# Kernel optimization log

Hardware: AMD Instinct MI355X
Metric: run time of the kernel (lower is better)

Reference implementation:

```python
import jax, jax.numpy as jnp
import numpy as np

DIM = 2048
N_HEADS = 32
N_KV_HEADS = 8
HEAD_DIM = DIM // N_HEADS  # 64
N_REP = N_HEADS // N_KV_HEADS
ROPE_BASE = 10000.0


def rope_tables(seq_len, dim):
    inv_freq = 1.0 / (ROPE_BASE ** (jnp.arange(0, dim, 2, dtype=jnp.float32) / dim))
    t = jnp.arange(seq_len, dtype=jnp.float32)
    freqs = jnp.outer(t, inv_freq)            # [S, dim/2]
    emb = jnp.concatenate([freqs, freqs], -1)  # [S, dim]
    return jnp.cos(emb), jnp.sin(emb)          # each [S, dim]


def rotate_half(x):
    x1, x2 = jnp.split(x, 2, axis=-1)
    return jnp.concatenate([-x2, x1], axis=-1)


def setup_inputs() -> dict:
    key = jax.random.key(0)
    k_x, k_q, k_k, k_v, k_o = jax.random.split(key, 5)
    B, S = 2, 2048
    scale = 0.02
    x = jax.random.normal(k_x, (B, S, DIM), dtype=jnp.float32)
    # torch Linear weights are [out, in]
    w_q = jax.random.normal(k_q, (N_HEADS * HEAD_DIM, DIM), dtype=jnp.float32) * scale
    w_k = jax.random.normal(k_k, (N_KV_HEADS * HEAD_DIM, DIM), dtype=jnp.float32) * scale
    w_v = jax.random.normal(k_v, (N_KV_HEADS * HEAD_DIM, DIM), dtype=jnp.float32) * scale
    w_o = jax.random.normal(k_o, (DIM, N_HEADS * HEAD_DIM), dtype=jnp.float32) * scale
    return {"x": x, "w_q": w_q, "w_k": w_k, "w_v": w_v, "w_o": w_o}


def reference(x, w_q, w_k, w_v, w_o):
    B, S, _ = x.shape
    # projections (torch Linear: x @ W^T), reshape to [B, H, S, D]
    q = jnp.einsum('bsd,ed->bse', x, w_q).reshape(B, S, N_HEADS, HEAD_DIM).transpose(0, 2, 1, 3)
    k = jnp.einsum('bsd,ed->bse', x, w_k).reshape(B, S, N_KV_HEADS, HEAD_DIM).transpose(0, 2, 1, 3)
    v = jnp.einsum('bsd,ed->bse', x, w_v).reshape(B, S, N_KV_HEADS, HEAD_DIM).transpose(0, 2, 1, 3)
    # RoPE
    cos, sin = rope_tables(S, HEAD_DIM)  # [S, D]
    cos = cos[None, None]
    sin = sin[None, None]
    q = q * cos + rotate_half(q) * sin
    k = k * cos + rotate_half(k) * sin
    # GQA: expand kv heads (repeat_interleave along head dim)
    k = jnp.repeat(k, N_REP, axis=1)
    v = jnp.repeat(v, N_REP, axis=1)
    # attention
    scores = jnp.einsum('bhqd,bhkd->bhqk', q, k) / jnp.sqrt(jnp.float32(HEAD_DIM))
    attn = jax.nn.softmax(scores, axis=-1)
    out = jnp.einsum('bhqk,bhkd->bhqd', attn, v)
    out = out.transpose(0, 2, 1, 3).reshape(B, S, N_HEADS * HEAD_DIM)
    return jnp.einsum('bse,de->bsd', out, w_o)
```

## Files before the change

### kernel.cpp

```cpp
#include <hip/hip_runtime.h>
#include <hip/hip_bf16.h>

typedef __attribute__((ext_vector_type(8))) short bf16x8;
typedef __attribute__((ext_vector_type(4))) short bf16x4s;
typedef __attribute__((ext_vector_type(4))) float f32x4;
typedef __attribute__((ext_vector_type(2))) unsigned int u32x2;
typedef unsigned int u32;

#define DIM 2048
#define NH 32
#define NKV 8
#define HD 64
#define BB 2
#define SS 2048
#define MROWS (BB*SS)
#define NQKV 3072
#define KDIM 2048
#define L2E 1.44269504f

__device__ __forceinline__ short f2bf(float f){
  u32 u = __float_as_uint(f);
  u32 r = u + 0x7fffu + ((u >> 16) & 1u);
  return (short)(r >> 16);
}
__device__ __forceinline__ float bf2f(short s){
  return __uint_as_float(((u32)(unsigned short)s) << 16);
}

__device__ __forceinline__ void gload16(const void* g, void* l){
  __builtin_amdgcn_global_load_lds((const __attribute__((address_space(1))) u32*)g,
                                   (__attribute__((address_space(3))) u32*)l, 16, 0, 0);
}

__global__ __launch_bounds__(256) void cvt_kernel(const float* __restrict__ in,
                                                  short* __restrict__ out, int n4){
  int i = blockIdx.x*256 + threadIdx.x;
  if (i >= n4) return;
  f32x4 v = ((const f32x4*)in)[i];
  bf16x4s o;
  #pragma unroll
  for (int j=0;j<4;++j) o[j] = f2bf(v[j]);
  ((bf16x4s*)out)[i] = o;
}

__global__ __launch_bounds__(256) void ropetab_kernel(float* __restrict__ cosT,
                                                      float* __restrict__ sinT){
  int idx = blockIdx.x*256 + threadIdx.x;
  if (idx >= SS*32) return;
  int s = idx >> 5, i = idx & 31;
  float inv = powf(10000.f, -(float)i * (1.f/32.f));
  float f = (float)s * inv;
  cosT[idx] = cosf(f);
  sinT[idx] = sinf(f);
}

__global__ __launch_bounds__(256) void rope_kernel(short* __restrict__ qkv,
                                                   const float* __restrict__ cosT,
                                                   const float* __restrict__ sinT){
  int idx = blockIdx.x*256 + threadIdx.x;
  int i = idx & 31;
  int rest = idx >> 5;
  int head = rest % 40;
  int m = rest / 40;
  if (m >= MROWS) return;
  int s = m & (SS-1);
  size_t base = (size_t)m*NQKV + head*64;
  float sc = (head < 32) ? 0.125f : 1.0f;
  float c  = cosT[(s<<5)+i], sn = sinT[(s<<5)+i];
  float x1 = bf2f(qkv[base+i]), x2 = bf2f(qkv[base+32+i]);
  qkv[base+i]    = f2bf((x1*c - x2*sn)*sc);
  qkv[base+32+i] = f2bf((x2*c + x1*sn)*sc);
}

__global__ __launch_bounds__(256) void vT_kernel(const short* __restrict__ qkv,
                                                 short* __restrict__ Vtg){
  __shared__ short T[64*72];
  const int tid = threadIdx.x;
  const int s0 = blockIdx.x*64, hkv = blockIdx.y, b = blockIdx.z;
  const short* vbase = qkv + (size_t)b*SS*NQKV + DIM + NKV*HD + hkv*HD;
  #pragma unroll
  for (int cc=0; cc<2; ++cc){
    int c = tid + cc*256;
    int s = c >> 3, dc = c & 7;
    bf16x8 v = *(const bf16x8*)(vbase + (size_t)(s0+s)*NQKV + dc*8);
    #pragma unroll
    for (int i=0;i<8;++i) T[(dc*8+i)*72 + s] = v[i];
  }
  __syncthreads();
  short* obase = Vtg + ((size_t)(b*NKV + hkv)*64)*SS;
  #pragma unroll
  for (int cc=0; cc<2; ++cc){
    int c = tid + cc*256;
    int d = c >> 3, sc = c & 7;
    *(bf16x8*)(obase + (size_t)d*SS + s0 + sc*8) = *(const bf16x8*)&T[d*72 + sc*8];
  }
}

__global__ __launch_bounds__(256) void gemm_bt_kernel(const short* __restrict__ A,
                                                      const short* __restrict__ Bm,
                                                      short* __restrict__ C,
                                                      int ldc, int K){
  __shared__ short As[128*32];
  __shared__ short Bs[128*32];
  const int tid = threadIdx.x;
  const int wave = tid >> 6, lane = tid & 63;
  const int g = lane >> 4, r16 = lane & 15;
  const int m0 = blockIdx.y * 128, n0 = blockIdx.x * 128;
  const int wr = wave >> 1, wc = wave & 1;
  f32x4 acc[4][4] = {};
  for (int k0 = 0; k0 < K; k0 += 32){
    #pragma unroll
    for (int c2 = 0; c2 < 2; ++c2){
      int ch = (wave*2 + c2)*64 + lane;
      int row = ch >> 2, kc = ch & 3;
      gload16(A  + (size_t)(m0+row)*K + k0 + kc*8, (char*)As + (wave*2+c2)*1024);
      gload16(Bm + (size_t)(n0+row)*K + k0 + kc*8, (char*)Bs + (wave*2+c2)*1024);
    }
    __syncthreads();
    bf16x8 a[4], b[4];
    #pragma unroll
    for (int i=0;i<4;++i)
      a[i] = *(const bf16x8*)&As[(wr*64 + i*16 + r16)*32 + g*8];
    #pragma unroll
    for (int j=0;j<4;++j)
      b[j] = *(const bf16x8*)&Bs[(wc*64 + j*16 + r16)*32 + g*8];
    #pragma unroll
    for (int i=0;i<4;++i)
      #pragma unroll
      for (int j=0;j<4;++j)
        acc[i][j] = __builtin_amdgcn_mfma_f32_16x16x32_bf16(a[i], b[j], acc[i][j], 0, 0, 0);
    __syncthreads();
  }
  #pragma unroll
  for (int i=0;i<4;++i)
    #pragma unroll
    for (int j=0;j<4;++j)
      #pragma unroll
      for (int r=0;r<4;++r){
        int row = m0 + wr*64 + i*16 + g*4 + r;
        int col = n0 + wc*64 + j*16 + r16;
        C[(size_t)row*ldc + col] = f2bf(acc[i][j][r]);
      }
}

__global__ __launch_bounds__(256) void gemm_btf_kernel(const short* __restrict__ A,
                                                       const short* __restrict__ Bm,
                                                       float* __restrict__ C,
                                                       int ldc, int K){
  __shared__ short As[128*32];
  __shared__ short Bs[128*32];
  const int tid = threadIdx.x;
  const int wave = tid >> 6, lane = tid & 63;
  const int g = lane >> 4, r16 = lane & 15;
  const int m0 = blockIdx.y * 128, n0 = blockIdx.x * 128;
  const int wr = wave >> 1, wc = wave & 1;
  f32x4 acc[4][4] = {};
  for (int k0 = 0; k0 < K; k0 += 32){
    #pragma unroll
    for (int c2 = 0; c2 < 2; ++c2){
      int ch = (wave*2 + c2)*64 + lane;
      int row = ch >> 2, kc = ch & 3;
      gload16(A  + (size_t)(m0+row)*K + k0 + kc*8, (char*)As + (wave*2+c2)*1024);
      gload16(Bm + (size_t)(n0+row)*K + k0 + kc*8, (char*)Bs + (wave*2+c2)*1024);
    }
    __syncthreads();
    bf16x8 a[4], b[4];
    #pragma unroll
    for (int i=0;i<4;++i)
      a[i] = *(const bf16x8*)&As[(wr*64 + i*16 + r16)*32 + g*8];
    #pragma unroll
    for (int j=0;j<4;++j)
      b[j] = *(const bf16x8*)&Bs[(wc*64 + j*16 + r16)*32 + g*8];
    #pragma unroll
    for (int i=0;i<4;++i)
      #pragma unroll
      for (int j=0;j<4;++j)
        acc[i][j] = __builtin_amdgcn_mfma_f32_16x16x32_bf16(a[i], b[j], acc[i][j], 0, 0, 0);
    __syncthreads();
  }
  #pragma unroll
  for (int i=0;i<4;++i)
    #pragma unroll
    for (int j=0;j<4;++j)
      #pragma unroll
      for (int r=0;r<4;++r){
        int row = m0 + wr*64 + i*16 + g*4 + r;
        int col = n0 + wc*64 + j*16 + r16;
        C[(size_t)row*ldc + col] = acc[i][j][r];
      }
}

__global__ __launch_bounds__(512) void attn_kernel(const short* __restrict__ qkv,
                                                   const short* __restrict__ Vtg,
                                                   short* __restrict__ outb){
  __shared__ short Ks[64*64];
  __shared__ short Vt[64*64];
  __shared__ short Ps[8*16*72];
  const int tid = threadIdx.x;
  const int wave = tid >> 6, lane = tid & 63;
  const int g = lane >> 4, r16 = lane & 15;
  const int qt = blockIdx.x, h = blockIdx.y, b = blockIdx.z;
  const int hkv = h >> 2;
  const size_t row0 = (size_t)b * SS;
  const int qrow0 = qt*128 + wave*16;
  const short* qbase  = qkv + (row0 + qrow0)*NQKV + h*HD;
  const short* kbase  = qkv + row0*NQKV + DIM + hkv*HD;
  const short* vtbase = Vtg + ((size_t)(b*NKV + hkv)*64)*SS;

  bf16x8 qf[2];
  #pragma unroll
  for (int kk=0;kk<2;++kk)
    qf[kk] = *(const bf16x8*)(qbase + (size_t)r16*NQKV + kk*32 + g*8);

  f32x4 oaccT[4] = {};
  float M = -6.0e29f;
  float lrow = 0.f;

  short* pwv = &Ps[wave*16*72];

  for (int s0 = 0; s0 < SS; s0 += 64){
    {
      int key = tid >> 3, c3 = tid & 7;
      gload16(kbase + (size_t)(s0+key)*NQKV + (((c3 ^ (key&7))) << 3),
              (char*)Ks + wave*1024);
      int d = tid >> 3;
      gload16(vtbase + (size_t)d*SS + s0 + (((c3 ^ (d&7))) << 3),
              (char*)Vt + wave*1024);
    }
    __syncthreads();

    f32x4 sacc[4];
    #pragma unroll
    for (int t=0;t<4;++t){
      f32x4 cacc = {};
      #pragma unroll
      for (int kk=0;kk<2;++kk){
        int row = t*16 + r16;
        const bf16x8* kp = (const bf16x8*)((const char*)Ks + row*128 +
                            ((((kk<<2)+g) ^ (row&7)) << 4));
        cacc = __builtin_amdgcn_mfma_f32_16x16x32_bf16(*kp, qf[kk], cacc, 0,0,0);
      }
      sacc[t] = cacc;
    }

    float mx = sacc[0][0];
    #pragma unroll
    for (int t=0;t<4;++t)
      #pragma unroll
      for (int r=0;r<4;++r) mx = fmaxf(mx, sacc[t][r]);
    mx = fmaxf(mx, __shfl_xor(mx, 16));
    mx = fmaxf(mx, __shfl_xor(mx, 32));
    float Mnew = fmaxf(M, mx * L2E);
    float al;
    { float a = M - Mnew; asm("v_exp_f32 %0, %1" : "=v"(al) : "v"(a)); }
    float sum = 0.f;
    u32 pb[4][2];
    #pragma unroll
    for (int t=0;t<4;++t){
      float p[4];
      #pragma unroll
      for (int r=0;r<4;++r){
        float a = fmaf(sacc[t][r], L2E, -Mnew);
        asm("v_exp_f32 %0, %1" : "=v"(p[r]) : "v"(a));
        sum += p[r];
      }
      asm("v_cvt_pk_bf16_f32 %0, %1, %2" : "=v"(pb[t][0]) : "v"(p[0]), "v"(p[1]));
      asm("v_cvt_pk_bf16_f32 %0, %1, %2" : "=v"(pb[t][1]) : "v"(p[2]), "v"(p[3]));
    }
    sum += __shfl_xor(sum, 16);
    sum += __shfl_xor(sum, 32);
    lrow = lrow*al + sum;
    M = Mnew;
    #pragma unroll
    for (int j=0;j<4;++j)
      #pragma unroll
      for (int r=0;r<4;++r) oaccT[j][r] *= al;
    #pragma unroll
    for (int t=0;t<4;++t)
      *(u32x2*)&pwv[r16*72 + t*16 + g*4] = (u32x2){pb[t][0], pb[t][1]};

    #pragma unroll
    for (int kk=0;kk<2;++kk){
      bf16x8 pf = *(const bf16x8*)&pwv[r16*72 + 32*kk + g*8];
      #pragma unroll
      for (int j=0;j<4;++j){
        int d = j*16 + r16;
        const bf16x8* vp = (const bf16x8*)((const char*)Vt + d*128 +
                            ((((kk<<2)+g) ^ (d&7)) << 4));
        oaccT[j] = __builtin_amdgcn_mfma_f32_16x16x32_bf16(*vp, pf, oaccT[j], 0,0,0);
      }
    }
    __syncthreads();
  }

  float inv = 1.0f / lrow;
  short* orow = outb + (row0 + qrow0 + r16)*(size_t)DIM + h*HD;
  #pragma unroll
  for (int j=0;j<4;++j){
    bf16x4s ov;
    #pragma unroll
    for (int r=0;r<4;++r) ov[r] = f2bf(oaccT[j][r]*inv);
    *(bf16x4s*)&orow[j*16 + g*4] = ov;
  }
}

extern "C" void kernel_launch(void* const* d_in, const int* in_sizes, int n_in,
                              void* d_out, int out_size, void* d_ws, size_t ws_size,
                              hipStream_t stream){
  const float* x  = (const float*)d_in[0];
  const float* wq = (const float*)d_in[1];
  const float* wk = (const float*)d_in[2];
  const float* wv = (const float*)d_in[3];
  const float* wo = (const float*)d_in[4];
  float* outf = (float*)d_out;

  char* ws = (char*)d_ws;
  short* wqkvb = (short*)(ws);
  short* attnb = (short*)(ws);
  short* wob   = (short*)(ws + 16777216);
  short* qkv   = (short*)(ws + 25165824);
  float* cosT  = (float*)(ws + 50331648);
  float* sinT  = (float*)(ws + 50593792);
  short* xb    = (short*)d_out;
  short* Vtg   = (short*)((char*)d_out + 16777216);

  cvt_kernel<<<(MROWS*KDIM/4+255)/256, 256, 0, stream>>>(x,  xb,    MROWS*KDIM/4);
  cvt_kernel<<<(2048*2048/4+255)/256, 256, 0, stream>>>(wq, wqkvb, 2048*2048/4);
  cvt_kernel<<<(512*2048/4+255)/256,  256, 0, stream>>>(wk, wqkvb + 2048*2048, 512*2048/4);
  cvt_kernel<<<(512*2048/4+255)/256,  256, 0, stream>>>(wv, wqkvb + 2560*2048, 512*2048/4);
  cvt_kernel<<<(2048*2048/4+255)/256, 256, 0, stream>>>(wo, wob,   2048*2048/4);
  ropetab_kernel<<<(SS*32+255)/256, 256, 0, stream>>>(cosT, sinT);

  gemm_bt_kernel<<<dim3(NQKV/128, MROWS/128), 256, 0, stream>>>(xb, wqkvb, qkv, NQKV, KDIM);
  rope_kernel<<<(MROWS*40*32)/256, 256, 0, stream>>>(qkv, cosT, sinT);
  vT_kernel<<<dim3(SS/64, NKV, BB), 256, 0, stream>>>(qkv, Vtg);
  attn_kernel<<<dim3(SS/128, NH, BB), 512, 0, stream>>>(qkv, Vtg, attnb);
  gemm_btf_kernel<<<dim3(DIM/128, MROWS/128), 256, 0, stream>>>(attnb, wob, outf, DIM, KDIM);
}
```

Measured before the change: 280.6 us.

## Fuse conversions, fold RoPE into QKV GEMM epilogue, widen attention key tiles

Merges the five fp32-to-bf16 conversion launches into one kernel and removes the separate RoPE pass by applying rotation and the Q scale in the QKV GEMM epilogue. The attention kernel now processes 128 keys per iteration with larger K/V LDS tiles and a wider swizzle. It also adds a lazy-rescale rule that updates the running max only when the new max exceeds the old by a threshold. This cuts launches and a full read/write of the QKV buffer, and halves barrier count in attention, at the cost of more LDS and registers per block. The lazy rescale relies on bounded exponent growth to stay accurate.

```diff
diff --git a/kernel.cpp b/kernel.cpp
--- a/kernel.cpp
+++ b/kernel.cpp
@@ -32,15 +32,28 @@
                                    (__attribute__((address_space(3))) u32*)l, 16, 0, 0);
 }
 
-__global__ __launch_bounds__(256) void cvt_kernel(const float* __restrict__ in,
-                                                  short* __restrict__ out, int n4){
-  int i = blockIdx.x*256 + threadIdx.x;
-  if (i >= n4) return;
-  f32x4 v = ((const f32x4*)in)[i];
+__global__ __launch_bounds__(256) void cvt_all_kernel(const float* __restrict__ x,
+                                                      const float* __restrict__ wq,
+                                                      const float* __restrict__ wk,
+                                                      const float* __restrict__ wv,
+                                                      const float* __restrict__ wo,
+                                                      short* __restrict__ xb,
+                                                      short* __restrict__ wqkvb,
+                                                      short* __restrict__ wob){
+  int bid = blockIdx.x;
+  int i = bid*256 + threadIdx.x;
+  const float* src; short* dst; int off;
+  if      (bid <  8192){ src = x;  dst = xb;              off = 0; }
+  else if (bid < 12288){ src = wq; dst = wqkvb;           off = 2097152; }
+  else if (bid < 13312){ src = wk; dst = wqkvb+2048*2048; off = 3145728; }
+  else if (bid < 14336){ src = wv; dst = wqkvb+2560*2048; off = 3407872; }
+  else                 { src = wo; dst = wob;             off = 3670016; }
+  int j = i - off;
+  f32x4 v = ((const f32x4*)src)[j];
   bf16x4s o;
   #pragma unroll
-  for (int j=0;j<4;++j) o[j] = f2bf(v[j]);
-  ((bf16x4s*)out)[i] = o;
+  for (int t=0;t<4;++t) o[t] = f2bf(v[t]);
+  ((bf16x4s*)dst)[j] = o;
 }
 
 __global__ __launch_bounds__(256) void ropetab_kernel(float* __restrict__ cosT,
@@ -54,24 +67,6 @@
   sinT[idx] = sinf(f);
 }
 
-__global__ __launch_bounds__(256) void rope_kernel(short* __restrict__ qkv,
-                                                   const float* __restrict__ cosT,
-                                                   const float* __restrict__ sinT){
-  int idx = blockIdx.x*256 + threadIdx.x;
-  int i = idx & 31;
-  int rest = idx >> 5;
-  int head = rest % 40;
-  int m = rest / 40;
-  if (m >= MROWS) return;
-  int s = m & (SS-1);
-  size_t base = (size_t)m*NQKV + head*64;
-  float sc = (head < 32) ? 0.125f : 1.0f;
-  float c  = cosT[(s<<5)+i], sn = sinT[(s<<5)+i];
-  float x1 = bf2f(qkv[base+i]), x2 = bf2f(qkv[base+32+i]);
-  qkv[base+i]    = f2bf((x1*c - x2*sn)*sc);
-  qkv[base+32+i] = f2bf((x2*c + x1*sn)*sc);
-}
-
 __global__ __launch_bounds__(256) void vT_kernel(const short* __restrict__ qkv,
                                                  short* __restrict__ Vtg){
   __shared__ short T[64*72];
@@ -99,7 +94,10 @@
 __global__ __launch_bounds__(256) void gemm_bt_kernel(const short* __restrict__ A,
                                                       const short* __restrict__ Bm,
                                                       short* __restrict__ C,
-                                                      int ldc, int K){
+                                                      int ldc, int K,
+                                                      const float* __restrict__ cosT,
+                                                      const float* __restrict__ sinT,
+                                                      int rope){
   __shared__ short As[128*32];
   __shared__ short Bs[128*32];
   const int tid = threadIdx.x;
@@ -131,16 +129,36 @@
         acc[i][j] = __builtin_amdgcn_mfma_f32_16x16x32_bf16(a[i], b[j], acc[i][j], 0, 0, 0);
     __syncthreads();
   }
-  #pragma unroll
-  for (int i=0;i<4;++i)
-    #pragma unroll
-    for (int j=0;j<4;++j)
+  if (rope && n0 < 2560){
+    float qsc = (n0 < 2048) ? 0.125f : 1.0f;
+    #pragma unroll
+    for (int i=0;i<4;++i)
       #pragma unroll
       for (int r=0;r<4;++r){
         int row = m0 + wr*64 + i*16 + g*4 + r;
-        int col = n0 + wc*64 + j*16 + r16;
-        C[(size_t)row*ldc + col] = f2bf(acc[i][j][r]);
-      }
+        int s = row & (SS-1);
+        #pragma unroll
+        for (int j=0;j<2;++j){
+          int col = n0 + wc*64 + j*16 + r16;
+          float c  = cosT[(s<<5) + (col&31)];
+          float sn = sinT[(s<<5) + (col&31)];
+          float x1 = acc[i][j][r], x2 = acc[i][j+2][r];
+          C[(size_t)row*ldc + col]      = f2bf((x1*c - x2*sn)*qsc);
+          C[(size_t)row*ldc + col + 32] = f2bf((x2*c + x1*sn)*qsc);
+        }
+      }
+  } else {
+    #pragma unroll
+    for (int i=0;i<4;++i)
+      #pragma unroll
+      for (int j=0;j<4;++j)
+        #pragma unroll
+        for (int r=0;r<4;++r){
+          int row = m0 + wr*64 + i*16 + g*4 + r;
+          int col = n0 + wc*64 + j*16 + r16;
+          C[(size_t)row*ldc + col] = f2bf(acc[i][j][r]);
+        }
+  }
 }
 
 __global__ __launch_bounds__(256) void gemm_btf_kernel(const short* __restrict__ A,
@@ -193,8 +211,8 @@
 __global__ __launch_bounds__(512) void attn_kernel(const short* __restrict__ qkv,
                                                    const short* __restrict__ Vtg,
                                                    short* __restrict__ outb){
-  __shared__ short Ks[64*64];
-  __shared__ short Vt[64*64];
+  __shared__ short Ks[128*64];
+  __shared__ short Vt[64*128];
   __shared__ short Ps[8*16*72];
   const int tid = threadIdx.x;
   const int wave = tid >> 6, lane = tid & 63;
@@ -218,26 +236,28 @@
 
   short* pwv = &Ps[wave*16*72];
 
-  for (int s0 = 0; s0 < SS; s0 += 64){
-    {
-      int key = tid >> 3, c3 = tid & 7;
-      gload16(kbase + (size_t)(s0+key)*NQKV + (((c3 ^ (key&7))) << 3),
-              (char*)Ks + wave*1024);
-      int d = tid >> 3;
-      gload16(vtbase + (size_t)d*SS + s0 + (((c3 ^ (d&7))) << 3),
-              (char*)Vt + wave*1024);
-    }
-    __syncthreads();
-
-    f32x4 sacc[4];
-    #pragma unroll
-    for (int t=0;t<4;++t){
+  for (int s0 = 0; s0 < SS; s0 += 128){
+    #pragma unroll
+    for (int c=0;c<2;++c){
+      int ch = tid + c*512;
+      int krow = ch >> 3, c3 = ch & 7;
+      gload16(kbase + (size_t)(s0+krow)*NQKV + ((c3 ^ (krow&7)) << 3),
+              (char*)Ks + c*8192 + wave*1024);
+      int d = ch >> 4, c16 = ch & 15;
+      gload16(vtbase + (size_t)d*SS + s0 + ((c16 ^ (d&15)) << 3),
+              (char*)Vt + c*8192 + wave*1024);
+    }
+    __syncthreads();
+
+    f32x4 sacc[8];
+    #pragma unroll
+    for (int t=0;t<8;++t){
       f32x4 cacc = {};
       #pragma unroll
       for (int kk=0;kk<2;++kk){
-        int row = t*16 + r16;
-        const bf16x8* kp = (const bf16x8*)((const char*)Ks + row*128 +
-                            ((((kk<<2)+g) ^ (row&7)) << 4));
+        int krow = t*16 + r16;
+        const bf16x8* kp = (const bf16x8*)((const char*)Ks + krow*128 +
+                            ((((kk<<2)+g) ^ (krow&7)) << 4));
         cacc = __builtin_amdgcn_mfma_f32_16x16x32_bf16(*kp, qf[kk], cacc, 0,0,0);
       }
       sacc[t] = cacc;
@@ -245,22 +265,31 @@
 
     float mx = sacc[0][0];
     #pragma unroll
-    for (int t=0;t<4;++t)
+    for (int t=0;t<8;++t)
       #pragma unroll
       for (int r=0;r<4;++r) mx = fmaxf(mx, sacc[t][r]);
     mx = fmaxf(mx, __shfl_xor(mx, 16));
     mx = fmaxf(mx, __shfl_xor(mx, 32));
-    float Mnew = fmaxf(M, mx * L2E);
-    float al;
-    { float a = M - Mnew; asm("v_exp_f32 %0, %1" : "=v"(al) : "v"(a)); }
+    float mxl = mx * L2E;
+    if (__any(mxl > M + 11.5f)){
+      float Mnew = fmaxf(M, mxl);
+      float al;
+      { float a = M - Mnew; asm("v_exp_f32 %0, %1" : "=v"(al) : "v"(a)); }
+      lrow *= al;
+      #pragma unroll
+      for (int j=0;j<4;++j)
+        #pragma unroll
+        for (int r=0;r<4;++r) oaccT[j][r] *= al;
+      M = Mnew;
+    }
     float sum = 0.f;
-    u32 pb[4][2];
-    #pragma unroll
-    for (int t=0;t<4;++t){
+    u32 pb[8][2];
+    #pragma unroll
+    for (int t=0;t<8;++t){
       float p[4];
       #pragma unroll
       for (int r=0;r<4;++r){
-        float a = fmaf(sacc[t][r], L2E, -Mnew);
+        float a = fmaf(sacc[t][r], L2E, -M);
         asm("v_exp_f32 %0, %1" : "=v"(p[r]) : "v"(a));
         sum += p[r];
       }
@@ -269,25 +298,24 @@
     }
     sum += __shfl_xor(sum, 16);
     sum += __shfl_xor(sum, 32);
-    lrow = lrow*al + sum;
-    M = Mnew;
-    #pragma unroll
-    for (int j=0;j<4;++j)
-      #pragma unroll
-      for (int r=0;r<4;++r) oaccT[j][r] *= al;
-    #pragma unroll
-    for (int t=0;t<4;++t)
-      *(u32x2*)&pwv[r16*72 + t*16 + g*4] = (u32x2){pb[t][0], pb[t][1]};
-
-    #pragma unroll
-    for (int kk=0;kk<2;++kk){
-      bf16x8 pf = *(const bf16x8*)&pwv[r16*72 + 32*kk + g*8];
-      #pragma unroll
-      for (int j=0;j<4;++j){
-        int d = j*16 + r16;
-        const bf16x8* vp = (const bf16x8*)((const char*)Vt + d*128 +
-                            ((((kk<<2)+g) ^ (d&7)) << 4));
-        oaccT[j] = __builtin_amdgcn_mfma_f32_16x16x32_bf16(*vp, pf, oaccT[j], 0,0,0);
+    lrow += sum;
+
+    #pragma unroll
+    for (int h2=0;h2<2;++h2){
+      #pragma unroll
+      for (int t2=0;t2<4;++t2)
+        *(u32x2*)&pwv[r16*72 + t2*16 + g*4] = (u32x2){pb[h2*4+t2][0], pb[h2*4+t2][1]};
+      #pragma unroll
+      for (int kki=0;kki<2;++kki){
+        bf16x8 pf = *(const bf16x8*)&pwv[r16*72 + 32*kki + g*8];
+        int kkg = h2*2 + kki;
+        #pragma unroll
+        for (int j=0;j<4;++j){
+          int d = j*16 + r16;
+          const bf16x8* vp = (const bf16x8*)((const char*)Vt + d*256 +
+                              ((((kkg<<2)+g) ^ (d&15)) << 4));
+          oaccT[j] = __builtin_amdgcn_mfma_f32_16x16x32_bf16(*vp, pf, oaccT[j], 0,0,0);
+        }
       }
     }
     __syncthreads();
@@ -324,15 +352,11 @@
   short* xb    = (short*)d_out;
   short* Vtg   = (short*)((char*)d_out + 16777216);
 
-  cvt_kernel<<<(MROWS*KDIM/4+255)/256, 256, 0, stream>>>(x,  xb,    MROWS*KDIM/4);
-  cvt_kernel<<<(2048*2048/4+255)/256, 256, 0, stream>>>(wq, wqkvb, 2048*2048/4);
-  cvt_kernel<<<(512*2048/4+255)/256,  256, 0, stream>>>(wk, wqkvb + 2048*2048, 512*2048/4);
-  cvt_kernel<<<(512*2048/4+255)/256,  256, 0, stream>>>(wv, wqkvb + 2560*2048, 512*2048/4);
-  cvt_kernel<<<(2048*2048/4+255)/256, 256, 0, stream>>>(wo, wob,   2048*2048/4);
-  ropetab_kernel<<<(SS*32+255)/256, 256, 0, stream>>>(cosT, sinT);
-
-  gemm_bt_kernel<<<dim3(NQKV/128, MROWS/128), 256, 0, stream>>>(xb, wqkvb, qkv, NQKV, KDIM);
-  rope_kernel<<<(MROWS*40*32)/256, 256, 0, stream>>>(qkv, cosT, sinT);
+  cvt_all_kernel<<<18432, 256, 0, stream>>>(x, wq, wk, wv, wo, xb, wqkvb, wob);
+  ropetab_kernel<<<256, 256, 0, stream>>>(cosT, sinT);
+
+  gemm_bt_kernel<<<dim3(NQKV/128, MROWS/128), 256, 0, stream>>>(xb, wqkvb, qkv, NQKV, KDIM,
+                                                                cosT, sinT, 1);
   vT_kernel<<<dim3(SS/64, NKV, BB), 256, 0, stream>>>(qkv, Vtg);
   attn_kernel<<<dim3(SS/128, NH, BB), 512, 0, stream>>>(qkv, Vtg, attnb);
   gemm_btf_kernel<<<dim3(DIM/128, MROWS/128), 256, 0, stream>>>(attnb, wob, outf, DIM, KDIM);
```

Result: faster. 251.2 us (-10.5%).
